# Kernel optimization log

Measured on AMD Instinct MI355X. Metric: run time of the kernel, lower is better.

Reference implementation:

```python
import jax, jax.numpy as jnp
import numpy as np

B, S, D = 64, 512, 1536  # D = 768*2 (last hidden concat layer-11 hidden)


def setup_inputs() -> dict:
    key = jax.random.key(0)
    ks = jax.random.split(key, 12)
    out_per_seq = jax.random.normal(ks[0], (B, S, D), dtype=jnp.float32)
    # entity span boundaries; spans are [loc+1, loc') as in the torch slices
    l0 = jax.random.randint(ks[1], (B, 1), 1, 20)
    l1 = l0 + jax.random.randint(ks[2], (B, 1), 2, 8)
    sep0 = jnp.full((B, 1), S // 2 - 1, dtype=jnp.int32)  # first [SEP]
    sep1 = sep0 + 1                                        # second [SEP]
    l2 = sep1 + jax.random.randint(ks[3], (B, 1), 1, 20)
    l3 = l2 + jax.random.randint(ks[4], (B, 1), 2, 8)
    locs = jnp.concatenate([l0, l1, l2, l3], axis=1).astype(jnp.int32)
    seps = jnp.concatenate([sep0, sep1], axis=1).astype(jnp.int32)
    sc = 0.02
    W_in = jax.random.normal(ks[5], (D, D), dtype=jnp.float32) * sc   # torchnlp Attention 'general' linear_in (no bias)
    W1 = jax.random.normal(ks[6], (1024, 4 * D), dtype=jnp.float32) * sc
    b1 = jax.random.normal(ks[7], (1024,), dtype=jnp.float32) * sc
    alpha = jnp.full((1,), 0.25, dtype=jnp.float32)                    # PReLU weight
    W2 = jax.random.normal(ks[8], (1, 1024), dtype=jnp.float32) * sc
    b2 = jax.random.normal(ks[9], (1,), dtype=jnp.float32) * sc
    return {"out_per_seq": out_per_seq, "W_in": W_in, "W1": W1, "b1": b1,
            "alpha": alpha, "W2": W2, "b2": b2, "locs": locs, "seps": seps}


def _masked_mean(x, mask):
    # x: [B,S,D], mask: [B,S] bool -> [B,D]
    m = mask.astype(x.dtype)
    return jnp.einsum("bs,bsd->bd", m, x) / jnp.sum(m, axis=1, keepdims=True)


def _attn_pool(entity, seq, mask, W_in):
    # torchnlp Attention('general'): scores = (entity @ W_in^T) . seq_j, softmax over
    # the ragged sub-sequence (mask), then attention-weighted sum of seq.
    q = entity @ W_in.T                                    # [B,D]
    scores = jnp.einsum("bd,bsd->bs", q, seq)              # [B,S]
    scores = jnp.where(mask, scores, -jnp.inf)
    w = jax.nn.softmax(scores, axis=-1)                    # [B,S]
    return jnp.einsum("bs,bsd->bd", w, seq)                # [B,D]


def reference(out_per_seq, W_in, W1, b1, alpha, W2, b2, locs, seps):
    idx = jnp.arange(S, dtype=jnp.int32)[None, :]          # [1,S]
    l0, l1, l2, l3 = (locs[:, k:k + 1] for k in range(4))  # each [B,1]
    sep0, sep1 = seps[:, 0:1], seps[:, 1:2]

    e1_mask = (idx > l0) & (idx < l1)                      # out[i, l0+1:l1]
    e2_mask = (idx > l2) & (idx < l3)                      # out[i, l2+1:l3]
    # imp_seq1 = out[i, 0:l0+1] ++ out[i, l1:sep0]
    imp1_mask = (idx <= l0) | ((idx >= l1) & (idx < sep0))
    # imp_seq2 = out[i, sep1:l2+1] ++ out[i, l3:]
    imp2_mask = ((idx >= sep1) & (idx <= l2)) | (idx >= l3)

    entity1 = _masked_mean(out_per_seq, e1_mask)
    entity2 = _masked_mean(out_per_seq, e2_mask)

    sent_attn2 = _attn_pool(entity2, out_per_seq, imp2_mask, W_in)
    sent_attn1 = _attn_pool(entity1, out_per_seq, imp1_mask, W_in)

    feat = jnp.concatenate([sent_attn2, sent_attn1, out_per_seq[:, 0], entity2], axis=-1)  # [B, 4D]
    h = feat @ W1.T + b1                                   # [B,1024]
    h = jnp.where(h >= 0, h, alpha * h)                    # PReLU (dropout=eval identity)
    return h @ W2.T + b2                                   # [B,1]
```

## Files before the change

kernel.cpp:

```cpp
#include <hip/hip_runtime.h>
#include <hip/hip_bf16.h>
#include <cmath>

#define NB 64
#define SS 512
#define DD 1536
#define DH 6144

#define WS_E     0
#define WS_Q     196608
#define WS_FEAT  589824
#define WS_PART  983040
#define WS_HPART 4145152
#define PSTR 1544

__device__ __forceinline__ float dot4(float4 a, float4 b) {
  return a.x * b.x + a.y * b.y + a.z * b.z + a.w * b.w;
}

__global__ __launch_bounds__(256) void k_entity(const float* __restrict__ x,
                                                const int* __restrict__ locs,
                                                float* __restrict__ ws) {
  const int seg = blockIdx.x;
  const int b = blockIdx.y;
  const int d = seg * 256 + threadIdx.x;
  const int l0 = locs[b * 4 + 0], l1 = locs[b * 4 + 1];
  const int l2 = locs[b * 4 + 2], l3 = locs[b * 4 + 3];
  const float* xb = x + (size_t)b * SS * DD;
  float s1 = 0.f, s2 = 0.f;
  for (int s = l0 + 1; s < l1; ++s) s1 += xb[(size_t)s * DD + d];
  for (int s = l2 + 1; s < l3; ++s) s2 += xb[(size_t)s * DD + d];
  const float e1 = s1 / (float)(l1 - l0 - 1);
  const float e2 = s2 / (float)(l3 - l2 - 1);
  ws[WS_E + (size_t)b * DD + d] = e1;
  ws[WS_E + (size_t)(NB + b) * DD + d] = e2;
  ws[WS_FEAT + (size_t)b * DH + 3072 + d] = xb[d];
  ws[WS_FEAT + (size_t)b * DH + 4608 + d] = e2;
}

__global__ __launch_bounds__(256) void k_qgemv(const float* __restrict__ Wm,
                                               float* __restrict__ ws) {
  const int bx = blockIdx.x;
  const int ks = bx / 192, r = bx % 192;
  const int vt = r & 7, nt = r >> 3;
  const int t = threadIdx.x, w = t >> 6, lane = t & 63;
  const int vi = lane >> 3, ni = lane & 7;
  const int v0 = vt * 16 + vi * 2;
  const int n0 = nt * 64 + w * 16 + ni * 2;
  const float4* e0p = (const float4*)(ws + WS_E + (size_t)v0 * DD) + ks * 192;
  const float4* e1p = (const float4*)(ws + WS_E + (size_t)(v0 + 1) * DD) + ks * 192;
  const float4* w0p = (const float4*)(Wm + (size_t)n0 * DD) + ks * 192;
  const float4* w1p = (const float4*)(Wm + (size_t)(n0 + 1) * DD) + ks * 192;
  float a00 = 0, a01 = 0, a10 = 0, a11 = 0;
#pragma unroll 2
  for (int k = 0; k < 192; ++k) {
    const float4 ea = e0p[k], eb = e1p[k];
    const float4 wa = w0p[k], wb = w1p[k];
    a00 += dot4(ea, wa); a01 += dot4(ea, wb);
    a10 += dot4(eb, wa); a11 += dot4(eb, wb);
  }
  float* q = ws + WS_Q + (size_t)ks * 196608;
  q[(size_t)v0 * DD + n0] = a00;
  q[(size_t)v0 * DD + n0 + 1] = a01;
  q[(size_t)(v0 + 1) * DD + n0] = a10;
  q[(size_t)(v0 + 1) * DD + n0 + 1] = a11;
}

__global__ __launch_bounds__(64, 4) void k_flash(const float* __restrict__ x,
                                                 const int* __restrict__ locs,
                                                 const int* __restrict__ seps,
                                                 float* __restrict__ ws) {
  const int bc = blockIdx.x;
  const int b = bc >> 5, c = bc & 31;
  const int pool = c >> 4;
  const int lane = threadIdx.x;
  const int l0 = locs[b * 4 + 0], l1 = locs[b * 4 + 1];
  const int l2 = locs[b * 4 + 2], l3 = locs[b * 4 + 3];
  const int sep0 = seps[b * 2 + 0], sep1 = seps[b * 2 + 1];
  const float* xb = x + (size_t)b * SS * DD;
  const float* q0 = ws + WS_Q + (size_t)(pool * NB + b) * DD;
  const float* q1 = q0 + 196608;
  float4 qf[6], acc[6];
#pragma unroll
  for (int j = 0; j < 6; ++j) {
    const float4 a = ((const float4*)q0)[lane + 64 * j];
    const float4 bq = ((const float4*)q1)[lane + 64 * j];
    qf[j] = make_float4(a.x + bq.x, a.y + bq.y, a.z + bq.z, a.w + bq.w);
    acc[j] = make_float4(0.f, 0.f, 0.f, 0.f);
  }
  float m = -INFINITY, l = 0.f;
  const int sbase = pool * 256 + (c & 15) * 16;
#pragma unroll 2
  for (int i = 0; i < 16; ++i) {
    const int s = sbase + i;
    const bool v = pool ? ((s >= sep1 && s <= l2) || s >= l3)
                        : (s <= l0 || (s >= l1 && s < sep0));
    if (!v) continue;
    const float4* xs = (const float4*)(xb + (size_t)s * DD);
    float4 xf[6];
#pragma unroll
    for (int j = 0; j < 6; ++j) xf[j] = xs[lane + 64 * j];
    float p = dot4(xf[0], qf[0]) + dot4(xf[1], qf[1]) + dot4(xf[2], qf[2]) +
              dot4(xf[3], qf[3]) + dot4(xf[4], qf[4]) + dot4(xf[5], qf[5]);
#pragma unroll
    for (int o = 1; o < 64; o <<= 1) p += __shfl_xor(p, o, 64);
    if (p <= m) {
      const float e = __expf(p - m);
      l += e;
#pragma unroll
      for (int j = 0; j < 6; ++j) {
        acc[j].x += e * xf[j].x; acc[j].y += e * xf[j].y;
        acc[j].z += e * xf[j].z; acc[j].w += e * xf[j].w;
      }
    } else {
      const float r = __expf(m - p);
      m = p; l = l * r + 1.f;
#pragma unroll
      for (int j = 0; j < 6; ++j) {
        acc[j].x = acc[j].x * r + xf[j].x; acc[j].y = acc[j].y * r + xf[j].y;
        acc[j].z = acc[j].z * r + xf[j].z; acc[j].w = acc[j].w * r + xf[j].w;
      }
    }
  }
  float* part = ws + WS_PART + (size_t)(b * 32 + c) * PSTR;
#pragma unroll
  for (int j = 0; j < 6; ++j) *(float4*)&part[4 * (lane + 64 * j)] = acc[j];
  if (lane == 0) { part[1536] = m; part[1537] = l; }
}

__global__ __launch_bounds__(256) void k_comb(float* __restrict__ ws) {
  const int bx = blockIdx.x;
  const int b = bx >> 1, pool = bx & 1;
  const int t = threadIdx.x;
  const float* base = ws + WS_PART + (size_t)(b * 32 + pool * 16) * PSTR;
  float ms[16];
  float mm = -INFINITY;
#pragma unroll
  for (int cc = 0; cc < 16; ++cc) {
    ms[cc] = base[cc * PSTR + 1536];
    mm = fmaxf(mm, ms[cc]);
  }
  float sc[16];
  float lsum = 0.f;
#pragma unroll
  for (int cc = 0; cc < 16; ++cc) {
    sc[cc] = __expf(ms[cc] - mm);
    lsum += base[cc * PSTR + 1537] * sc[cc];
  }
  const float inv = 1.f / lsum;
  const int off = pool ? 0 : 1536;
  float* feat = ws + WS_FEAT + (size_t)b * DH + off;
#pragma unroll
  for (int jj = 0; jj < 6; ++jj) {
    const int col = t + 256 * jj;
    float v = 0.f;
#pragma unroll
    for (int cc = 0; cc < 16; ++cc) v += base[cc * PSTR + col] * sc[cc];
    feat[col] = v * inv;
  }
}

__global__ __launch_bounds__(256) void k_mlp(const float* __restrict__ W1,
                                             float* __restrict__ ws) {
  __shared__ float lds[16384];
  const int bx = blockIdx.x;
  const int nt = bx & 63, ks = bx >> 6;
  const int t = threadIdx.x, w = t >> 6, lane = t & 63;
  const int ln = lane >> 4, lk = lane & 15;
  const int n = nt * 16 + w * 4 + ln;
  const int kb0 = ks * 1536;
  float acc[64];
#pragma unroll
  for (int b = 0; b < 64; ++b) acc[b] = 0.f;
  const float* feat = ws + WS_FEAT;
  for (int step = 0; step < 6; ++step) {
    const int kb = kb0 + step * 256;
    __syncthreads();
#pragma unroll
    for (int jj = 0; jj < 16; ++jj) {
      const int f = t + 256 * jj;
      const int row = f >> 6, c4 = f & 63;
      *(float4*)&lds[row * 256 + 4 * c4] =
          *(const float4*)&feat[(size_t)row * DH + kb + 4 * c4];
    }
    __syncthreads();
    const float* wr = W1 + (size_t)n * DH + kb + 4 * lk;
    const float4 w0 = *(const float4*)(wr);
    const float4 w1 = *(const float4*)(wr + 64);
    const float4 w2 = *(const float4*)(wr + 128);
    const float4 w3 = *(const float4*)(wr + 192);
#pragma unroll
    for (int b = 0; b < 64; ++b) {
      const float* lb = &lds[b * 256 + 4 * lk];
      const float4 f0 = *(const float4*)(lb);
      const float4 f1 = *(const float4*)(lb + 64);
      const float4 f2 = *(const float4*)(lb + 128);
      const float4 f3 = *(const float4*)(lb + 192);
      acc[b] += dot4(f0, w0) + dot4(f1, w1) + dot4(f2, w2) + dot4(f3, w3);
    }
  }
  __syncthreads();
#pragma unroll
  for (int i = 0; i < 16; ++i) {
    *(float4*)&lds[t * 64 + 4 * ((i ^ lk) & 15)] =
        make_float4(acc[4 * i], acc[4 * i + 1], acc[4 * i + 2], acc[4 * i + 3]);
  }
  __syncthreads();
  float4 h = make_float4(0.f, 0.f, 0.f, 0.f);
#pragma unroll
  for (int kp = 0; kp < 16; ++kp) {
    const float4 v =
        *(const float4*)&lds[(w * 64 + ln * 16 + kp) * 64 + 4 * ((lk ^ kp) & 15)];
    h.x += v.x; h.y += v.y; h.z += v.z; h.w += v.w;
  }
  *(float4*)&ws[WS_HPART + ((size_t)ks * 1024 + n) * 64 + 4 * lk] = h;
}

__global__ __launch_bounds__(256) void k_out(const float* __restrict__ b1,
                                             const float* __restrict__ alpha,
                                             const float* __restrict__ W2,
                                             const float* __restrict__ b2,
                                             const float* __restrict__ ws,
                                             float* __restrict__ out) {
  const int b = blockIdx.x;
  const int t = threadIdx.x;
  const float al = alpha[0];
  float partial = 0.f;
#pragma unroll
  for (int u = 0; u < 4; ++u) {
    const int n = t + 256 * u;
    float hs = 0.f;
#pragma unroll
    for (int ksp = 0; ksp < 4; ++ksp)
      hs += ws[WS_HPART + ((size_t)ksp * 1024 + n) * 64 + b];
    float h = hs + b1[n];
    h = (h >= 0.f) ? h : al * h;
    partial += h * W2[n];
  }
#pragma unroll
  for (int o = 1; o < 64; o <<= 1) partial += __shfl_xor(partial, o, 64);
  __shared__ float wsum[4];
  if ((t & 63) == 0) wsum[t >> 6] = partial;
  __syncthreads();
  if (t == 0) out[b] = b2[0] + wsum[0] + wsum[1] + wsum[2] + wsum[3];
}

extern "C" void kernel_launch(void* const* d_in, const int* in_sizes, int n_in,
                              void* d_out, int out_size, void* d_ws, size_t ws_size,
                              hipStream_t stream) {
  const float* x     = (const float*)d_in[0];
  const float* Wm    = (const float*)d_in[1];
  const float* W1    = (const float*)d_in[2];
  const float* b1    = (const float*)d_in[3];
  const float* alpha = (const float*)d_in[4];
  const float* W2    = (const float*)d_in[5];
  const float* b2    = (const float*)d_in[6];
  const int* locs    = (const int*)d_in[7];
  const int* seps    = (const int*)d_in[8];
  float* out = (float*)d_out;
  float* ws = (float*)d_ws;

  hipLaunchKernelGGL(k_entity, dim3(6, 64), dim3(256), 0, stream, x, locs, ws);
  hipLaunchKernelGGL(k_qgemv, dim3(384), dim3(256), 0, stream, Wm, ws);
  hipLaunchKernelGGL(k_flash, dim3(NB * 32), dim3(64), 0, stream, x, locs, seps, ws);
  hipLaunchKernelGGL(k_comb, dim3(NB * 2), dim3(256), 0, stream, ws);
  hipLaunchKernelGGL(k_mlp, dim3(256), dim3(256), 0, stream, W1, ws);
  hipLaunchKernelGGL(k_out, dim3(NB), dim3(256), 0, stream, b1, alpha, W2, b2, ws, out);
}
```

Before: 486.8 us.

## Process two rows per flash step and retile MLP GEMM with batch tiles and split-K by eight

The flash-attention loop now loads and scores two sequence rows per iteration without branching. Masked rows get -inf scores instead of being skipped, and the running max starts at a finite sentinel so masked-out chunks stay NaN-free. The MLP GEMM is retiled so each thread handles 4 output rows for 16 batch entries, with 512 blocks doing split-K over 8 slices, and the partial-sum layout changes to match k_out. The aim is more memory-level parallelism in flash and more W1 reuse in the MLP. The cost is higher register pressure (launch bounds lowered to 2) and flash now loading masked rows it used to skip.

```diff
diff --git a/kernel.cpp b/kernel.cpp
--- a/kernel.cpp
+++ b/kernel.cpp
@@ -66,7 +66,7 @@
   q[(size_t)(v0 + 1) * DD + n0 + 1] = a11;
 }
 
-__global__ __launch_bounds__(64, 4) void k_flash(const float* __restrict__ x,
+__global__ __launch_bounds__(64, 2) void k_flash(const float* __restrict__ x,
                                                  const int* __restrict__ locs,
                                                  const int* __restrict__ seps,
                                                  float* __restrict__ ws) {
@@ -88,38 +88,44 @@
     qf[j] = make_float4(a.x + bq.x, a.y + bq.y, a.z + bq.z, a.w + bq.w);
     acc[j] = make_float4(0.f, 0.f, 0.f, 0.f);
   }
-  float m = -INFINITY, l = 0.f;
+  float m = -1e30f, l = 0.f;
   const int sbase = pool * 256 + (c & 15) * 16;
 #pragma unroll 2
-  for (int i = 0; i < 16; ++i) {
-    const int s = sbase + i;
-    const bool v = pool ? ((s >= sep1 && s <= l2) || s >= l3)
-                        : (s <= l0 || (s >= l1 && s < sep0));
-    if (!v) continue;
-    const float4* xs = (const float4*)(xb + (size_t)s * DD);
-    float4 xf[6];
-#pragma unroll
-    for (int j = 0; j < 6; ++j) xf[j] = xs[lane + 64 * j];
-    float p = dot4(xf[0], qf[0]) + dot4(xf[1], qf[1]) + dot4(xf[2], qf[2]) +
-              dot4(xf[3], qf[3]) + dot4(xf[4], qf[4]) + dot4(xf[5], qf[5]);
-#pragma unroll
-    for (int o = 1; o < 64; o <<= 1) p += __shfl_xor(p, o, 64);
-    if (p <= m) {
-      const float e = __expf(p - m);
-      l += e;
-#pragma unroll
-      for (int j = 0; j < 6; ++j) {
-        acc[j].x += e * xf[j].x; acc[j].y += e * xf[j].y;
-        acc[j].z += e * xf[j].z; acc[j].w += e * xf[j].w;
-      }
-    } else {
-      const float r = __expf(m - p);
-      m = p; l = l * r + 1.f;
-#pragma unroll
-      for (int j = 0; j < 6; ++j) {
-        acc[j].x = acc[j].x * r + xf[j].x; acc[j].y = acc[j].y * r + xf[j].y;
-        acc[j].z = acc[j].z * r + xf[j].z; acc[j].w = acc[j].w * r + xf[j].w;
-      }
+  for (int i = 0; i < 16; i += 2) {
+    const int s0 = sbase + i;
+    const int s1 = s0 + 1;
+    const bool va = pool ? ((s0 >= sep1 && s0 <= l2) || s0 >= l3)
+                         : (s0 <= l0 || (s0 >= l1 && s0 < sep0));
+    const bool vb = pool ? ((s1 >= sep1 && s1 <= l2) || s1 >= l3)
+                         : (s1 <= l0 || (s1 >= l1 && s1 < sep0));
+    const float4* xsa = (const float4*)(xb + (size_t)s0 * DD);
+    const float4* xsb = (const float4*)(xb + (size_t)s1 * DD);
+    float4 xa[6], xc[6];
+#pragma unroll
+    for (int j = 0; j < 6; ++j) { xa[j] = xsa[lane + 64 * j]; xc[j] = xsb[lane + 64 * j]; }
+    float pa = dot4(xa[0], qf[0]) + dot4(xa[1], qf[1]) + dot4(xa[2], qf[2]) +
+               dot4(xa[3], qf[3]) + dot4(xa[4], qf[4]) + dot4(xa[5], qf[5]);
+    float pb = dot4(xc[0], qf[0]) + dot4(xc[1], qf[1]) + dot4(xc[2], qf[2]) +
+               dot4(xc[3], qf[3]) + dot4(xc[4], qf[4]) + dot4(xc[5], qf[5]);
+#pragma unroll
+    for (int o = 1; o < 64; o <<= 1) {
+      pa += __shfl_xor(pa, o, 64);
+      pb += __shfl_xor(pb, o, 64);
+    }
+    pa = va ? pa : -INFINITY;
+    pb = vb ? pb : -INFINITY;
+    const float mn = fmaxf(m, fmaxf(pa, pb));
+    const float r = __expf(m - mn);
+    const float ea = __expf(pa - mn);
+    const float eb = __expf(pb - mn);
+    m = mn;
+    l = l * r + ea + eb;
+#pragma unroll
+    for (int j = 0; j < 6; ++j) {
+      acc[j].x = acc[j].x * r + ea * xa[j].x + eb * xc[j].x;
+      acc[j].y = acc[j].y * r + ea * xa[j].y + eb * xc[j].y;
+      acc[j].z = acc[j].z * r + ea * xa[j].z + eb * xc[j].z;
+      acc[j].w = acc[j].w * r + ea * xa[j].w + eb * xc[j].w;
     }
   }
   float* part = ws + WS_PART + (size_t)(b * 32 + c) * PSTR;
@@ -134,7 +140,7 @@
   const int t = threadIdx.x;
   const float* base = ws + WS_PART + (size_t)(b * 32 + pool * 16) * PSTR;
   float ms[16];
-  float mm = -INFINITY;
+  float mm = -1e30f;
 #pragma unroll
   for (int cc = 0; cc < 16; ++cc) {
     ms[cc] = base[cc * PSTR + 1536];
@@ -162,58 +168,66 @@
 
 __global__ __launch_bounds__(256) void k_mlp(const float* __restrict__ W1,
                                              float* __restrict__ ws) {
-  __shared__ float lds[16384];
+  __shared__ float lds[16704];
   const int bx = blockIdx.x;
-  const int nt = bx & 63, ks = bx >> 6;
+  const int bt = bx & 3, nt = (bx >> 2) & 15, ks = bx >> 6;
   const int t = threadIdx.x, w = t >> 6, lane = t & 63;
-  const int ln = lane >> 4, lk = lane & 15;
-  const int n = nt * 16 + w * 4 + ln;
-  const int kb0 = ks * 1536;
-  float acc[64];
-#pragma unroll
-  for (int b = 0; b < 64; ++b) acc[b] = 0.f;
+  const int lk = lane & 15, ln = lane >> 4;
+  const int n0 = nt * 64 + w * 16 + ln * 4;
+  const int kb0 = ks * 768;
   const float* feat = ws + WS_FEAT;
-  for (int step = 0; step < 6; ++step) {
+  float acc[16][4];
+#pragma unroll
+  for (int b = 0; b < 16; ++b)
+#pragma unroll
+    for (int r = 0; r < 4; ++r) acc[b][r] = 0.f;
+
+  for (int step = 0; step < 3; ++step) {
     const int kb = kb0 + step * 256;
     __syncthreads();
 #pragma unroll
-    for (int jj = 0; jj < 16; ++jj) {
-      const int f = t + 256 * jj;
-      const int row = f >> 6, c4 = f & 63;
+    for (int j = 0; j < 4; ++j) {
+      const int idx = t + 256 * j;
+      const int row = idx >> 6, c4 = idx & 63;
       *(float4*)&lds[row * 256 + 4 * c4] =
-          *(const float4*)&feat[(size_t)row * DH + kb + 4 * c4];
+          *(const float4*)&feat[(size_t)(bt * 16 + row) * DH + kb + 4 * c4];
     }
     __syncthreads();
-    const float* wr = W1 + (size_t)n * DH + kb + 4 * lk;
-    const float4 w0 = *(const float4*)(wr);
-    const float4 w1 = *(const float4*)(wr + 64);
-    const float4 w2 = *(const float4*)(wr + 128);
-    const float4 w3 = *(const float4*)(wr + 192);
-#pragma unroll
-    for (int b = 0; b < 64; ++b) {
+    float4 wf[4][4];
+#pragma unroll
+    for (int r = 0; r < 4; ++r)
+#pragma unroll
+      for (int i = 0; i < 4; ++i)
+        wf[r][i] = *(const float4*)&W1[(size_t)(n0 + r) * DH + kb + i * 64 + 4 * lk];
+#pragma unroll
+    for (int b = 0; b < 16; ++b) {
       const float* lb = &lds[b * 256 + 4 * lk];
       const float4 f0 = *(const float4*)(lb);
       const float4 f1 = *(const float4*)(lb + 64);
       const float4 f2 = *(const float4*)(lb + 128);
       const float4 f3 = *(const float4*)(lb + 192);
-      acc[b] += dot4(f0, w0) + dot4(f1, w1) + dot4(f2, w2) + dot4(f3, w3);
+#pragma unroll
+      for (int r = 0; r < 4; ++r)
+        acc[b][r] += dot4(f0, wf[r][0]) + dot4(f1, wf[r][1]) +
+                     dot4(f2, wf[r][2]) + dot4(f3, wf[r][3]);
     }
   }
   __syncthreads();
-#pragma unroll
-  for (int i = 0; i < 16; ++i) {
-    *(float4*)&lds[t * 64 + 4 * ((i ^ lk) & 15)] =
-        make_float4(acc[4 * i], acc[4 * i + 1], acc[4 * i + 2], acc[4 * i + 3]);
-  }
+  float* R = &lds[w * 4176];
+#pragma unroll
+  for (int b = 0; b < 16; ++b)
+    *(float4*)&R[lk * 260 + b * 16 + ln * 4] =
+        make_float4(acc[b][0], acc[b][1], acc[b][2], acc[b][3]);
   __syncthreads();
   float4 h = make_float4(0.f, 0.f, 0.f, 0.f);
 #pragma unroll
-  for (int kp = 0; kp < 16; ++kp) {
-    const float4 v =
-        *(const float4*)&lds[(w * 64 + ln * 16 + kp) * 64 + 4 * ((lk ^ kp) & 15)];
+  for (int k2 = 0; k2 < 16; ++k2) {
+    const float4 v = *(const float4*)&R[k2 * 260 + lane * 4];
     h.x += v.x; h.y += v.y; h.z += v.z; h.w += v.w;
   }
-  *(float4*)&ws[WS_HPART + ((size_t)ks * 1024 + n) * 64 + 4 * lk] = h;
+  const int bo = bt * 16 + (lane >> 2);
+  const int no = nt * 64 + w * 16 + ((lane * 4) & 15);
+  *(float4*)&ws[WS_HPART + ((size_t)ks * 64 + bo) * 1024 + no] = h;
 }
 
 __global__ __launch_bounds__(256) void k_out(const float* __restrict__ b1,
@@ -231,8 +245,8 @@
     const int n = t + 256 * u;
     float hs = 0.f;
 #pragma unroll
-    for (int ksp = 0; ksp < 4; ++ksp)
-      hs += ws[WS_HPART + ((size_t)ksp * 1024 + n) * 64 + b];
+    for (int ksp = 0; ksp < 8; ++ksp)
+      hs += ws[WS_HPART + ((size_t)ksp * 64 + b) * 1024 + n];
     float h = hs + b1[n];
     h = (h >= 0.f) ? h : al * h;
     partial += h * W2[n];
@@ -264,6 +278,6 @@
   hipLaunchKernelGGL(k_qgemv, dim3(384), dim3(256), 0, stream, Wm, ws);
   hipLaunchKernelGGL(k_flash, dim3(NB * 32), dim3(64), 0, stream, x, locs, seps, ws);
   hipLaunchKernelGGL(k_comb, dim3(NB * 2), dim3(256), 0, stream, ws);
-  hipLaunchKernelGGL(k_mlp, dim3(256), dim3(256), 0, stream, W1, ws);
+  hipLaunchKernelGGL(k_mlp, dim3(512), dim3(256), 0, stream, W1, ws);
   hipLaunchKernelGGL(k_out, dim3(NB), dim3(256), 0, stream, b1, alpha, W2, b2, ws, out);
 }
```

Result: faster. 448.7 us (-7.8%).
